# Kernel tuning notes

Hardware: AMD Instinct MI355X
Metric: run time of the kernel (lower is better)

The kernel has to match this reference:

```python
import jax, jax.numpy as jnp
import numpy as np

EPS = 1e-12  # matches tf.math.l2_normalize epsilon

def _l2n(x, axis=-1):
    return x * jax.lax.rsqrt(jnp.maximum(jnp.sum(x * x, axis=axis, keepdims=True), EPS))


def setup_inputs() -> dict:
    key = jax.random.key(0)
    ks = jax.random.split(key, 8)
    B, T, D, N, M = 16, 1024, 1024, 2048, 256
    s = 1.0 / np.sqrt(D)
    return {
        "memory": jax.random.normal(ks[0], (N, M), jnp.float32),
        "controller_output": jax.random.normal(ks[1], (B, T, D), jnp.float32),
        "Wk": jax.random.normal(ks[2], (D, M), jnp.float32) * s,
        "bk": jnp.zeros((M,), jnp.float32),
        "We": jax.random.normal(ks[3], (D, M), jnp.float32) * s,
        "be": jnp.zeros((M,), jnp.float32),
        "Wa": jax.random.normal(ks[4], (D, M), jnp.float32) * s,
        "ba": jnp.zeros((M,), jnp.float32),
    }


def reference(memory, controller_output, Wk, bk, We, be, Wa, ba):
    B, T, _ = controller_output.shape
    # key: softmax over memory_size dim  -> [B,T,M]
    key = jax.nn.softmax(controller_output @ Wk + bk, axis=-1)
    # tf.keras.losses.cosine_similarity returns NEGATIVE cosine similarity
    kn = _l2n(key)          # [B,T,M]
    mn = _l2n(memory)       # [N,M]
    sims = -jnp.einsum('btm,nm->btn', kn, mn)          # [B,T,N]
    w = jax.nn.softmax(sims, axis=-1)                  # [B,T,N]
    erase = jax.nn.sigmoid(controller_output @ We + be)  # [B,T,M]
    add = jax.nn.relu(controller_output @ Wa + ba)       # [B,T,M]
    # mean over (B,T) of (1 - w*erase)*memory + w*add, without tiling memory:
    inv_bt = 1.0 / (B * T)
    we = jnp.einsum('btn,btm->nm', w, erase) * inv_bt   # mean of w \otimes erase
    wa = jnp.einsum('btn,btm->nm', w, add) * inv_bt     # mean of w \otimes add
    return memory * (1.0 - we) + wa                      # [N,M]
```

## Files before the change

### kernel.cpp

```cpp
#include <hip/hip_runtime.h>

#define DEV __device__ __forceinline__

using f32x4    = __attribute__((ext_vector_type(4))) float;
using bf16x8   = __attribute__((ext_vector_type(8))) short;
using float4_t = __attribute__((ext_vector_type(4))) float;
using ushort4_t = __attribute__((ext_vector_type(4))) unsigned short;
using ushort8_t = __attribute__((ext_vector_type(8))) unsigned short;

DEV unsigned short f2bf(float f) {
    unsigned int u = __builtin_bit_cast(unsigned int, f);
    u = (u + 0x7fffu + ((u >> 16) & 1u)) >> 16;
    return (unsigned short)u;
}
DEV float bf2f(unsigned short h) {
    unsigned int u = ((unsigned int)h) << 16;
    return __builtin_bit_cast(float, u);
}

DEV void gload_lds16(const void* g, void* l) {
    __builtin_amdgcn_global_load_lds((const __attribute__((address_space(1))) void*)g,
                                     (__attribute__((address_space(3))) void*)l, 16, 0, 0);
}

template<int TR, int TC, int NTH>
DEV void stage_tile(const unsigned short* __restrict__ src, long ld, long r0, long c0,
                    unsigned short* lds, int tid) {
    constexpr int LPR = (TC * 2) / 16;
    constexpr int RPI = 64 / LPR;
    constexpr int NISSUE = TR / RPI;
    constexpr int NW = NTH / 64;
    const int wid = tid >> 6, lane = tid & 63;
    const int lr = lane / LPR;
    const int lc = (lane % LPR) ^ lr;
#pragma unroll
    for (int ii = 0; ii < NISSUE / NW; ++ii) {
        const int i = ii * NW + wid;
        const long row = r0 + (long)i * RPI + lr;
        const unsigned short* g = src + row * ld + c0 + lc * 8;
        gload_lds16(g, lds + i * 512);
    }
}

__global__ void k0_cast_co(const float* __restrict__ in, unsigned short* __restrict__ out, long n4) {
    long i = (long)blockIdx.x * 256 + threadIdx.x;
    if (i >= n4) return;
    float4_t v = ((const float4_t*)in)[i];
    ushort4_t o;
#pragma unroll
    for (int j = 0; j < 4; ++j) o[j] = f2bf(v[j]);
    ((ushort4_t*)out)[i] = o;
}

__global__ void k0_prep_w(const float* __restrict__ Wk, const float* __restrict__ We,
                          const float* __restrict__ Wa, unsigned short* __restrict__ WcatT) {
    long idx = (long)blockIdx.x * 256 + threadIdx.x;
    int j = (int)(idx >> 10), d = (int)(idx & 1023);
    const float* W = (j < 256) ? Wk : (j < 512) ? We : Wa;
    int m = j & 255;
    WcatT[idx] = f2bf(W[(long)d * 256 + m]);
}

__global__ __launch_bounds__(256) void k0_mn(const float* __restrict__ memory,
                                             unsigned short* __restrict__ mn,
                                             float* __restrict__ S, int BT) {
    int gid = blockIdx.x * 256 + threadIdx.x;
    if (gid < BT) S[gid] = 0.f;
    int row = blockIdx.x * 4 + (threadIdx.x >> 6);
    int lane = threadIdx.x & 63;
    float4_t v = ((const float4_t*)(memory + (long)row * 256))[lane];
    float ss = v[0]*v[0] + v[1]*v[1] + v[2]*v[2] + v[3]*v[3];
#pragma unroll
    for (int d = 1; d < 64; d <<= 1) ss += __shfl_xor(ss, d);
    float sc = rsqrtf(fmaxf(ss, 1e-12f));
    ushort4_t o;
#pragma unroll
    for (int j = 0; j < 4; ++j) o[j] = f2bf(v[j] * sc);
    ((ushort4_t*)(mn + (long)row * 256))[lane] = o;
}

template<int BM, int BN, int BK>
__global__ __launch_bounds__(512, 4)
void k1_fused(const unsigned short* __restrict__ A, const unsigned short* __restrict__ BT,
              const float* __restrict__ bk, const float* __restrict__ be,
              const float* __restrict__ ba, unsigned short* __restrict__ kn,
              unsigned short* __restrict__ er, unsigned short* __restrict__ ad, int K) {
    __shared__ __align__(16) unsigned short As[BM * BK];
    __shared__ __align__(16) unsigned short Bs[BN * BK];
    const int tid = threadIdx.x, lane = tid & 63, wid = tid >> 6;
    const long m0 = (long)blockIdx.x * BM;
    const int y = blockIdx.y;
    const int wrg = wid >> 2, wcg = wid & 3;
    const int wr = wrg * 64, wc = wcg * 64;
    const int c16 = lane & 15, rq = (lane >> 4) * 4, swz = (lane & 7) * 8;
    f32x4 acc[4][4] = {};
    for (int kt = 0; kt < K; kt += BK) {
        stage_tile<BM, BK, 512>(A, K, m0, kt, As, tid);
        stage_tile<BN, BK, 512>(BT, K, (long)y * BN, kt, Bs, tid);
        __syncthreads();
#pragma unroll
        for (int kk = 0; kk < BK; kk += 32) {
            const int klo = kk + (lane >> 4) * 8;
            bf16x8 af[4], bfr[4];
#pragma unroll
            for (int i = 0; i < 4; ++i) {
                af[i]  = *(const bf16x8*)&As[((wr + i * 16 + c16) * BK + klo) ^ swz];
                bfr[i] = *(const bf16x8*)&Bs[((wc + i * 16 + c16) * BK + klo) ^ swz];
            }
#pragma unroll
            for (int i = 0; i < 4; ++i)
#pragma unroll
                for (int j = 0; j < 4; ++j)
                    acc[i][j] = __builtin_amdgcn_mfma_f32_16x16x32_bf16(af[i], bfr[j], acc[i][j], 0, 0, 0);
        }
        __syncthreads();
    }
    const float* bias = (y == 0) ? bk : (y == 1) ? be : ba;
    float bj[4];
#pragma unroll
    for (int j = 0; j < 4; ++j) bj[j] = bias[wc + j * 16 + c16];

    if (y == 0) {
        float* redsm = (float*)As;
#pragma unroll
        for (int i = 0; i < 4; ++i) {
            float p[4] = {0.f, 0.f, 0.f, 0.f};
#pragma unroll
            for (int j = 0; j < 4; ++j)
#pragma unroll
                for (int r = 0; r < 4; ++r) {
                    float e = __expf(acc[i][j][r] + bj[j]);
                    acc[i][j][r] = e;
                    p[r] += e * e;
                }
#pragma unroll
            for (int d = 1; d < 16; d <<= 1)
#pragma unroll
                for (int r = 0; r < 4; ++r) p[r] += __shfl_xor(p[r], d);
            if (c16 == 0) {
#pragma unroll
                for (int r = 0; r < 4; ++r)
                    redsm[(wrg * 4 + wcg) * 64 + i * 16 + rq + r] = p[r];
            }
        }
        __syncthreads();
#pragma unroll
        for (int i = 0; i < 4; ++i)
#pragma unroll
            for (int r = 0; r < 4; ++r) {
                const int row64 = i * 16 + rq + r;
                float tot = redsm[(wrg * 4 + 0) * 64 + row64] + redsm[(wrg * 4 + 1) * 64 + row64]
                          + redsm[(wrg * 4 + 2) * 64 + row64] + redsm[(wrg * 4 + 3) * 64 + row64];
                float sc = rsqrtf(tot);
                const long row = m0 + wr + row64;
#pragma unroll
                for (int j = 0; j < 4; ++j)
                    kn[row * 256 + wc + j * 16 + c16] = f2bf(acc[i][j][r] * sc);
            }
    } else {
        unsigned short* dst = (y == 1) ? er : ad;
#pragma unroll
        for (int i = 0; i < 4; ++i)
#pragma unroll
            for (int r = 0; r < 4; ++r) {
                const long row = m0 + wr + i * 16 + rq + r;
#pragma unroll
                for (int j = 0; j < 4; ++j) {
                    float v = acc[i][j][r] + bj[j];
                    float o = (y == 1) ? 1.f / (1.f + __expf(-v)) : fmaxf(v, 0.f);
                    dst[row * 256 + wc + j * 16 + c16] = f2bf(o);
                }
            }
    }
}

template<int BM, int BN, int BK>
__global__ __launch_bounds__(256, 4)
void k3_gemm_sims(const unsigned short* __restrict__ A, const unsigned short* __restrict__ BT,
                  unsigned short* __restrict__ ET, float* __restrict__ S,
                  int M, int N, int K) {
    __shared__ __align__(16) unsigned short smem[BN * (BM + 8)];
    unsigned short* As = smem;
    unsigned short* Bs = smem + BM * BK;
    const int tid = threadIdx.x, lane = tid & 63, wid = tid >> 6;
    const long m0 = (long)blockIdx.x * BM, n0 = (long)blockIdx.y * BN;
    const int wr = (wid >> 1) * 64, wc = (wid & 1) * 64;
    const int c16 = lane & 15, rq = (lane >> 4) * 4, swz = (lane & 7) * 8;
    f32x4 acc[4][4] = {};
    for (int kt = 0; kt < K; kt += BK) {
        stage_tile<BM, BK, 256>(A, K, m0, kt, As, tid);
        stage_tile<BN, BK, 256>(BT, K, n0, kt, Bs, tid);
        __syncthreads();
#pragma unroll
        for (int kk = 0; kk < BK; kk += 32) {
            const int klo = kk + (lane >> 4) * 8;
            bf16x8 af[4], bfr[4];
#pragma unroll
            for (int i = 0; i < 4; ++i) {
                af[i]  = *(const bf16x8*)&As[((wr + i * 16 + c16) * BK + klo) ^ swz];
                bfr[i] = *(const bf16x8*)&Bs[((wc + i * 16 + c16) * BK + klo) ^ swz];
            }
#pragma unroll
            for (int i = 0; i < 4; ++i)
#pragma unroll
                for (int j = 0; j < 4; ++j)
                    acc[i][j] = __builtin_amdgcn_mfma_f32_16x16x32_bf16(af[i], bfr[j], acc[i][j], 0, 0, 0);
        }
        __syncthreads();
    }
    float rs[4][4];
#pragma unroll
    for (int i = 0; i < 4; ++i)
#pragma unroll
        for (int r = 0; r < 4; ++r) rs[i][r] = 0.f;
#pragma unroll
    for (int i = 0; i < 4; ++i) {
#pragma unroll
        for (int j = 0; j < 4; ++j) {
            ushort4_t pk;
#pragma unroll
            for (int r = 0; r < 4; ++r) {
                float e = __expf(-acc[i][j][r]);
                rs[i][r] += e;
                pk[r] = f2bf(e);
            }
            *(ushort4_t*)&smem[(wc + j * 16 + c16) * (BM + 8) + wr + i * 16 + rq] = pk;
        }
    }
#pragma unroll
    for (int d = 1; d < 16; d <<= 1)
#pragma unroll
        for (int i = 0; i < 4; ++i)
#pragma unroll
            for (int r = 0; r < 4; ++r) rs[i][r] += __shfl_xor(rs[i][r], d);
    if (c16 == 0) {
#pragma unroll
        for (int i = 0; i < 4; ++i)
#pragma unroll
            for (int r = 0; r < 4; ++r)
                atomicAdd(&S[m0 + wr + i * 16 + rq + r], rs[i][r]);
    }
    __syncthreads();
    constexpr int CPR = BM / 8;
#pragma unroll
    for (int it = 0; it < (BN * CPR) / 256; ++it) {
        int flat = it * 256 + tid;
        int c = flat / CPR, ch = flat % CPR;
        *(ushort8_t*)&ET[(n0 + c) * (long)M + m0 + ch * 8] =
            *(const ushort8_t*)&smem[c * (BM + 8) + ch * 8];
    }
}

__global__ __launch_bounds__(256) void k3c_scale_transpose(
        const unsigned short* __restrict__ er, const unsigned short* __restrict__ ad,
        const float* __restrict__ S, unsigned short* __restrict__ cat,
        float inv_bt, int BTr) {
    const unsigned short* src = blockIdx.y ? ad : er;
    unsigned short* dst = cat + (blockIdx.y ? (long)256 * BTr : 0);
    __shared__ __align__(16) unsigned short Tl[64][256 + 8];
    const int tid = threadIdx.x;
    const long kbase = (long)blockIdx.x * 64;
#pragma unroll
    for (int it = 0; it < 8; ++it) {
        int flat = it * 2048 + tid * 8;
        int kl = flat >> 8, m = flat & 255;
        float scale = inv_bt / S[kbase + kl];
        ushort8_t v = *(const ushort8_t*)&src[(kbase + kl) * 256 + m];
        ushort8_t o;
#pragma unroll
        for (int j = 0; j < 8; ++j) o[j] = f2bf(bf2f(v[j]) * scale);
        *(ushort8_t*)&Tl[kl][m] = o;
    }
    __syncthreads();
#pragma unroll
    for (int it = 0; it < 8; ++it) {
        int flat = it * 2048 + tid * 8;
        int m = flat >> 6, kc = flat & 63;
        ushort8_t o;
#pragma unroll
        for (int j = 0; j < 8; ++j) o[j] = Tl[kc + j][m];
        *(ushort8_t*)&dst[(long)m * BTr + kbase + kc] = o;
    }
}

template<int BM, int BN, int BK>
__global__ __launch_bounds__(512, 4)
void k4_gemm_cat(const unsigned short* __restrict__ A, const unsigned short* __restrict__ Bc,
                 unsigned short* __restrict__ pP, long Ktot, int Kchunk) {
    __shared__ __align__(16) unsigned short As[BM * BK];
    __shared__ __align__(16) unsigned short Bs[BN * BK];
    const int tid = threadIdx.x, lane = tid & 63, wid = tid >> 6;
    const long n0 = (long)blockIdx.x * BM;
    const long mc0 = (long)blockIdx.y * BN;
    const int sk = blockIdx.z;
    const long kbeg = (long)sk * Kchunk;
    const int wr = (wid >> 1) * 64, wc = (wid & 1) * 64;
    const int c16 = lane & 15, rq = (lane >> 4) * 4, swz = (lane & 7) * 8;
    f32x4 acc[4][4] = {};
    for (int kt = 0; kt < Kchunk; kt += BK) {
        stage_tile<BM, BK, 512>(A, Ktot, n0, kbeg + kt, As, tid);
        stage_tile<BN, BK, 512>(Bc, Ktot, mc0, kbeg + kt, Bs, tid);
        __syncthreads();
#pragma unroll
        for (int kk = 0; kk < BK; kk += 32) {
            const int klo = kk + (lane >> 4) * 8;
            bf16x8 af[4], bfr[4];
#pragma unroll
            for (int i = 0; i < 4; ++i) {
                af[i]  = *(const bf16x8*)&As[((wr + i * 16 + c16) * BK + klo) ^ swz];
                bfr[i] = *(const bf16x8*)&Bs[((wc + i * 16 + c16) * BK + klo) ^ swz];
            }
#pragma unroll
            for (int i = 0; i < 4; ++i)
#pragma unroll
                for (int j = 0; j < 4; ++j)
                    acc[i][j] = __builtin_amdgcn_mfma_f32_16x16x32_bf16(af[i], bfr[j], acc[i][j], 0, 0, 0);
        }
        __syncthreads();
    }
#pragma unroll
    for (int i = 0; i < 4; ++i) {
        const long row = n0 + wr + i * 16 + rq;
#pragma unroll
        for (int j = 0; j < 4; ++j) {
            const long col = mc0 + wc + j * 16 + c16;
#pragma unroll
            for (int r = 0; r < 4; ++r)
                pP[((long)sk * 2048 + row + r) * 512 + col] = f2bf(acc[i][j][r]);
        }
    }
}

__global__ __launch_bounds__(256) void k5_finalize(const float* __restrict__ mem,
                                                   const unsigned short* __restrict__ pP,
                                                   float* __restrict__ out, int splits) {
    int idx = blockIdx.x * 256 + threadIdx.x;
    int n = idx >> 6, m4 = (idx & 63) * 4;
    float we[4] = {0.f, 0.f, 0.f, 0.f}, wa[4] = {0.f, 0.f, 0.f, 0.f};
    for (int s = 0; s < splits; ++s) {
        const unsigned short* row = pP + ((long)s * 2048 + n) * 512;
        ushort4_t ve = *(const ushort4_t*)&row[m4];
        ushort4_t va = *(const ushort4_t*)&row[256 + m4];
#pragma unroll
        for (int j = 0; j < 4; ++j) { we[j] += bf2f(ve[j]); wa[j] += bf2f(va[j]); }
    }
    float4_t mv = ((const float4_t*)mem)[idx];
    float4_t o;
#pragma unroll
    for (int j = 0; j < 4; ++j) o[j] = mv[j] * (1.f - we[j]) + wa[j];
    ((float4_t*)out)[idx] = o;
}

extern "C" void kernel_launch(void* const* d_in, const int* in_sizes, int n_in,
                              void* d_out, int out_size, void* d_ws, size_t ws_size,
                              hipStream_t stream) {
    const float* memory = (const float*)d_in[0];
    const float* co     = (const float*)d_in[1];
    const float* Wk     = (const float*)d_in[2];
    const float* bk     = (const float*)d_in[3];
    const float* We     = (const float*)d_in[4];
    const float* be     = (const float*)d_in[5];
    const float* Wa     = (const float*)d_in[6];
    const float* ba     = (const float*)d_in[7];
    float* out = (float*)d_out;

    constexpr int BT = 16384, D = 1024, N = 2048, NC = 768;
    constexpr int SPLITK = 16;

    char* ws = (char*)d_ws;
    unsigned short* co_bf  = (unsigned short*)(ws + 0);
    unsigned short* ET     = (unsigned short*)(ws + 0);
    unsigned short* kn     = (unsigned short*)(ws + 67108864);
    unsigned short* er     = (unsigned short*)(ws + 75497472);
    unsigned short* ad     = (unsigned short*)(ws + 83886080);
    unsigned short* mn     = (unsigned short*)(ws + 92274688);
    unsigned short* WcatT  = (unsigned short*)(ws + 93323264);
    float*          Sbuf   = (float*)(ws + 94896128);
    unsigned short* cat    = (unsigned short*)(ws + 94961664);
    unsigned short* pP     = (unsigned short*)(ws + 111738880);

    k0_cast_co<<<(BT * (long)D / 4) / 256, 256, 0, stream>>>(co, co_bf, BT * (long)D / 4);
    k0_prep_w<<<(NC * D) / 256, 256, 0, stream>>>(Wk, We, Wa, WcatT);
    k0_mn<<<N / 4, 256, 0, stream>>>(memory, mn, Sbuf, BT);

    k1_fused<128, 256, 64><<<dim3(BT / 128, 3), 512, 0, stream>>>(
        co_bf, WcatT, bk, be, ba, kn, er, ad, D);

    k3_gemm_sims<128, 128, 64><<<dim3(BT / 128, N / 128), 256, 0, stream>>>(
        kn, mn, ET, Sbuf, BT, N, 256);

    k3c_scale_transpose<<<dim3(BT / 64, 2), 256, 0, stream>>>(
        er, ad, Sbuf, cat, 1.f / (float)BT, BT);

    k4_gemm_cat<256, 128, 64><<<dim3(N / 256, 512 / 128, SPLITK), 512, 0, stream>>>(
        ET, cat, pP, (long)BT, BT / SPLITK);

    k5_finalize<<<(N * 256 / 4) / 256, 256, 0, stream>>>(memory, pP, out, SPLITK);
}
```

Baseline: 239.8 us.

## Fuse fp32-to-bf16 cast of controller output into the projection GEMM A-tile load

Removes the standalone kernel that converted the 64MB fp32 controller output to bf16. The projection GEMM now reads fp32 directly, converts in registers and writes swizzled bf16 into LDS. The weight-transpose and memory-normalise prep kernels are also merged into one launch. This drops a 64MB read plus a 32MB write and one extra read pass. In exchange each GEMM block (3 along y) now reads fp32 A, doubling A bytes per block, synchronous loads replace async global-to-LDS copies, and launch bounds drop to 3 waves per SIMD.

```diff
diff --git a/kernel.cpp b/kernel.cpp
--- a/kernel.cpp
+++ b/kernel.cpp
@@ -42,46 +42,58 @@
     }
 }
 
-__global__ void k0_cast_co(const float* __restrict__ in, unsigned short* __restrict__ out, long n4) {
-    long i = (long)blockIdx.x * 256 + threadIdx.x;
-    if (i >= n4) return;
-    float4_t v = ((const float4_t*)in)[i];
-    ushort4_t o;
-#pragma unroll
-    for (int j = 0; j < 4; ++j) o[j] = f2bf(v[j]);
-    ((ushort4_t*)out)[i] = o;
-}
-
-__global__ void k0_prep_w(const float* __restrict__ Wk, const float* __restrict__ We,
-                          const float* __restrict__ Wa, unsigned short* __restrict__ WcatT) {
-    long idx = (long)blockIdx.x * 256 + threadIdx.x;
-    int j = (int)(idx >> 10), d = (int)(idx & 1023);
-    const float* W = (j < 256) ? Wk : (j < 512) ? We : Wa;
-    int m = j & 255;
-    WcatT[idx] = f2bf(W[(long)d * 256 + m]);
-}
-
-__global__ __launch_bounds__(256) void k0_mn(const float* __restrict__ memory,
-                                             unsigned short* __restrict__ mn,
-                                             float* __restrict__ S, int BT) {
-    int gid = blockIdx.x * 256 + threadIdx.x;
-    if (gid < BT) S[gid] = 0.f;
-    int row = blockIdx.x * 4 + (threadIdx.x >> 6);
-    int lane = threadIdx.x & 63;
-    float4_t v = ((const float4_t*)(memory + (long)row * 256))[lane];
-    float ss = v[0]*v[0] + v[1]*v[1] + v[2]*v[2] + v[3]*v[3];
-#pragma unroll
-    for (int d = 1; d < 64; d <<= 1) ss += __shfl_xor(ss, d);
-    float sc = rsqrtf(fmaxf(ss, 1e-12f));
-    ushort4_t o;
-#pragma unroll
-    for (int j = 0; j < 4; ++j) o[j] = f2bf(v[j] * sc);
-    ((ushort4_t*)(mn + (long)row * 256))[lane] = o;
+DEV void stage_A_f32(const float* __restrict__ src, long ld, long r0, long c0,
+                     unsigned short* lds, int tid) {
+#pragma unroll
+    for (int s = 0; s < 2; ++s) {
+        const int flat = s * 512 + tid;
+        const int row = flat >> 3, c = flat & 7;
+        const float* g = src + (r0 + row) * ld + c0 + c * 8;
+        float4_t v0 = *(const float4_t*)g;
+        float4_t v1 = *(const float4_t*)(g + 4);
+        ushort8_t o;
+#pragma unroll
+        for (int j = 0; j < 4; ++j) { o[j] = f2bf(v0[j]); o[4 + j] = f2bf(v1[j]); }
+        const int sc = c ^ (row & 7);
+        *(ushort8_t*)&lds[(row * 8 + sc) * 8] = o;
+    }
+}
+
+__global__ __launch_bounds__(256) void k0_prep(const float* __restrict__ Wk,
+                                               const float* __restrict__ We,
+                                               const float* __restrict__ Wa,
+                                               const float* __restrict__ memory,
+                                               unsigned short* __restrict__ WcatT,
+                                               unsigned short* __restrict__ mn,
+                                               float* __restrict__ S, int BT) {
+    const int b = blockIdx.x;
+    if (b < 3072) {
+        long idx = (long)b * 256 + threadIdx.x;
+        int j = (int)(idx >> 10), d = (int)(idx & 1023);
+        const float* W = (j < 256) ? Wk : (j < 512) ? We : Wa;
+        int m = j & 255;
+        WcatT[idx] = f2bf(W[(long)d * 256 + m]);
+    } else {
+        const int bb = b - 3072;
+        int gid = bb * 256 + threadIdx.x;
+        if (gid < BT) S[gid] = 0.f;
+        int row = bb * 4 + (threadIdx.x >> 6);
+        int lane = threadIdx.x & 63;
+        float4_t v = ((const float4_t*)(memory + (long)row * 256))[lane];
+        float ss = v[0]*v[0] + v[1]*v[1] + v[2]*v[2] + v[3]*v[3];
+#pragma unroll
+        for (int d = 1; d < 64; d <<= 1) ss += __shfl_xor(ss, d);
+        float sc = rsqrtf(fmaxf(ss, 1e-12f));
+        ushort4_t o;
+#pragma unroll
+        for (int j = 0; j < 4; ++j) o[j] = f2bf(v[j] * sc);
+        ((ushort4_t*)(mn + (long)row * 256))[lane] = o;
+    }
 }
 
 template<int BM, int BN, int BK>
-__global__ __launch_bounds__(512, 4)
-void k1_fused(const unsigned short* __restrict__ A, const unsigned short* __restrict__ BT,
+__global__ __launch_bounds__(512, 3)
+void k1_fused(const float* __restrict__ A, const unsigned short* __restrict__ BT,
               const float* __restrict__ bk, const float* __restrict__ be,
               const float* __restrict__ ba, unsigned short* __restrict__ kn,
               unsigned short* __restrict__ er, unsigned short* __restrict__ ad, int K) {
@@ -95,8 +107,8 @@
     const int c16 = lane & 15, rq = (lane >> 4) * 4, swz = (lane & 7) * 8;
     f32x4 acc[4][4] = {};
     for (int kt = 0; kt < K; kt += BK) {
-        stage_tile<BM, BK, 512>(A, K, m0, kt, As, tid);
         stage_tile<BN, BK, 512>(BT, K, (long)y * BN, kt, Bs, tid);
+        stage_A_f32(A, K, m0, kt, As, tid);
         __syncthreads();
 #pragma unroll
         for (int kk = 0; kk < BK; kk += 32) {
@@ -364,11 +376,10 @@
     const float* ba     = (const float*)d_in[7];
     float* out = (float*)d_out;
 
-    constexpr int BT = 16384, D = 1024, N = 2048, NC = 768;
+    constexpr int BT = 16384, D = 1024, N = 2048;
     constexpr int SPLITK = 16;
 
     char* ws = (char*)d_ws;
-    unsigned short* co_bf  = (unsigned short*)(ws + 0);
     unsigned short* ET     = (unsigned short*)(ws + 0);
     unsigned short* kn     = (unsigned short*)(ws + 67108864);
     unsigned short* er     = (unsigned short*)(ws + 75497472);
@@ -379,12 +390,10 @@
     unsigned short* cat    = (unsigned short*)(ws + 94961664);
     unsigned short* pP     = (unsigned short*)(ws + 111738880);
 
-    k0_cast_co<<<(BT * (long)D / 4) / 256, 256, 0, stream>>>(co, co_bf, BT * (long)D / 4);
-    k0_prep_w<<<(NC * D) / 256, 256, 0, stream>>>(Wk, We, Wa, WcatT);
-    k0_mn<<<N / 4, 256, 0, stream>>>(memory, mn, Sbuf, BT);
+    k0_prep<<<3072 + N / 4, 256, 0, stream>>>(Wk, We, Wa, memory, WcatT, mn, Sbuf, BT);
 
     k1_fused<128, 256, 64><<<dim3(BT / 128, 3), 512, 0, stream>>>(
-        co_bf, WcatT, bk, be, ba, kn, er, ad, D);
+        co, WcatT, bk, be, ba, kn, er, ad, D);
 
     k3_gemm_sims<128, 128, 64><<<dim3(BT / 128, N / 128), 256, 0, stream>>>(
         kn, mn, ET, Sbuf, BT, N, 256);
```

Result: faster. 231.0 us (-3.7%).
